# Kernel tuning notes

Measured on AMD Instinct MI355X. Metric: run time of the kernel, lower is better.

The kernel has to match this reference:

```python
import jax, jax.numpy as jnp
import numpy as np
from jax import lax

# STE sign: forward maps x>=0 -> +1, x<0 -> -1 (matches XORQuantizeSTE)
@jax.custom_vjp
def ste_sign(x):
    return jnp.where(x >= 0, jnp.ones_like(x), -jnp.ones_like(x))

def _ste_fwd(x):
    return ste_sign(x), None

def _ste_bwd(_, g):
    return (g,)  # identity pass-through

ste_sign.defvjp(_ste_fwd, _ste_bwd)


def _xor_quant(x, w):
    """Per-layer XNOR-Net quantization: alpha = mean|W| scales both
    binarized activation and binarized weight (as in the wrapper's hook
    + binarization())."""
    alpha = jnp.mean(jnp.abs(w))
    return alpha * ste_sign(x), alpha * ste_sign(w)


def _conv(x, w, b, stride):
    y = lax.conv_general_dilated(
        x, w, window_strides=(stride, stride), padding=((1, 1), (1, 1)),
        dimension_numbers=('NCHW', 'OIHW', 'NCHW'))
    return y + b[None, :, None, None]


def setup_inputs() -> dict:
    key = jax.random.key(0)
    ks = jax.random.split(key, 9)
    f32 = jnp.float32
    x = jax.random.normal(ks[0], (32, 3, 224, 224), dtype=f32)
    w1 = jax.random.normal(ks[1], (64, 3, 3, 3), dtype=f32) * 0.1
    b1 = jax.random.normal(ks[2], (64,), dtype=f32) * 0.01
    w2 = jax.random.normal(ks[3], (128, 64, 3, 3), dtype=f32) * 0.05
    b2 = jax.random.normal(ks[4], (128,), dtype=f32) * 0.01
    w3 = jax.random.normal(ks[5], (256, 128, 3, 3), dtype=f32) * 0.03
    b3 = jax.random.normal(ks[6], (256,), dtype=f32) * 0.01
    wf = jax.random.normal(ks[7], (1000, 256), dtype=f32) * 0.05
    bf = jax.random.normal(ks[8], (1000,), dtype=f32) * 0.01
    return {'x': x, 'w1': w1, 'b1': b1, 'w2': w2, 'b2': b2,
            'w3': w3, 'b3': b3, 'wf': wf, 'bf': bf}


def reference(x, w1, b1, w2, b2, w3, b3, wf, bf):
    # layer 1: binarize activation + weight with shared alpha, dense conv
    xq, wq = _xor_quant(x, w1)
    h = jnp.clip(_conv(xq, wq, b1, 2), -1.0, 1.0)   # [32,64,112,112]
    xq, wq = _xor_quant(h, w2)
    h = jnp.clip(_conv(xq, wq, b2, 2), -1.0, 1.0)   # [32,128,56,56]
    xq, wq = _xor_quant(h, w3)
    h = jnp.clip(_conv(xq, wq, b3, 2), -1.0, 1.0)   # [32,256,28,28]
    h = jnp.mean(h, axis=(2, 3))                     # global avg pool [32,256]
    xq, wq = _xor_quant(h, wf)
    return xq @ wq.T + bf                            # [32,1000]
```

## Files before the change

### kernel.cpp

```cpp
#include <hip/hip_runtime.h>
#include <stdint.h>
#include <math.h>


#define WP2_OFF    2048ull
#define WP3T_OFF   16384ull
#define WFP_OFF    65536ull
#define PART_OFF   100352ull
#define P1_OFF     102400ull
#define P2_OFF     3313664ull
#define POOLP_OFF  4919296ull

__global__ __launch_bounds__(256) void k1_conv1_pack(
    const float* __restrict__ x,  const float* __restrict__ w1, const float* __restrict__ b1,
    const float* __restrict__ w2, const float* __restrict__ w3, const float* __restrict__ wf,
    uint64_t* __restrict__ wp2, uint64_t* __restrict__ wp3t, uint64_t* __restrict__ wfp,
    double* __restrict__ part, uint64_t* __restrict__ p1)
{
    const int tid = threadIdx.x, lane = tid & 63, wid = tid >> 6, bid = blockIdx.x;
    if (bid < 896) {
        __shared__ float4   xf4[1512];
        __shared__ uint32_t xb[216];
        __shared__ uint32_t wm[64];
        __shared__ int      Ts[64];
        __shared__ double   a2s;
        const float* xf = (const float*)xf4;

        int n = bid / 28, hb = bid % 28;
        int ho0 = hb * 4;
        int hi0 = 2 * ho0 - 1;

        if (wid == 0) {
            double s = 0.0;
            #pragma unroll
            for (int i = 0; i < 27; i++) s += fabs((double)w1[lane + i*64]);
            #pragma unroll
            for (int off = 1; off < 64; off <<= 1) s += __shfl_xor(s, off, 64);
            if (lane == 0) { double a = s / 1728.0; a2s = a * a; }
        } else if (wid == 1) {
            uint32_t m = 0;
            for (int t = 0; t < 27; t++) {
                int ci = t / 9, r = t % 9, kh = r / 3, kw = r % 3;
                if (w1[((lane*3 + ci)*3 + kh)*3 + kw] >= 0.f) m |= (1u << t);
            }
            wm[lane] = m;
        }
        const float4* xg = (const float4*)x;
        for (int i = tid; i < 1512; i += 256) {
            int seg = i / 56, f4 = i % 56;
            int ci = seg / 9, r = seg % 9;
            int hi = hi0 + r;
            float4 v = make_float4(0.f, 0.f, 0.f, 0.f);
            if ((unsigned)hi < 224u) v = xg[((n*3 + ci)*224 + hi)*56 + f4];
            xf4[i] = v;
        }
        __syncthreads();
        if (tid < 64) {
            double a2 = a2s, b = (double)b1[tid];
            int k = (int)ceil(-b / a2);
            k = max(-27, min(28, k));
            while (k > -27 && (a2 * (double)(k - 1) + b >= 0.0)) k--;
            while (k <= 27 && !(a2 * (double)k + b >= 0.0)) k++;
            Ts[tid] = k;
        }
        if (tid < 189) {
            int seg = tid / 7, j = tid % 7;
            uint32_t u = 0;
            #pragma unroll
            for (int k = 0; k < 32; k++) {
                int o = (k + tid) & 31;
                if (xf[seg*224 + j*32 + o] >= 0.f) u |= (1u << o);
            }
            xb[seg*8 + j] = u;
        } else if (tid < 216) {
            xb[(tid - 189)*8 + 7] = 0u;
        }
        __syncthreads();

        for (int pass = 0; pass < 2; pass++) {
            int s = tid + pass*256;
            if (s >= 448) break;
            int dho = s / 112, wo = s % 112;
            int hop = ho0 + dho;
            uint32_t vm = 0x7FFFFFFu;
            if (hop == 0) vm &= ~0x1C0E07u;
            if (wo == 0)  vm &= ~0x1249249u;
            int c0 = 2*wo - 1;
            uint32_t xm = 0;
            if (wo > 0) {
                int w0 = c0 >> 5, sh = c0 & 31;
                #pragma unroll
                for (int ci = 0; ci < 3; ci++)
                    #pragma unroll
                    for (int kh = 0; kh < 3; kh++) {
                        int seg = ci*9 + 2*dho + kh;
                        uint64_t dw = (uint64_t)xb[seg*8 + w0]
                                    | ((uint64_t)xb[seg*8 + w0 + 1] << 32);
                        xm |= (uint32_t)((dw >> sh) & 7u) << (ci*9 + kh*3);
                    }
            } else {
                #pragma unroll
                for (int ci = 0; ci < 3; ci++)
                    #pragma unroll
                    for (int kh = 0; kh < 3; kh++) {
                        int seg = ci*9 + 2*dho + kh;
                        xm |= ((xb[seg*8] << 1) & 6u) << (ci*9 + kh*3);
                    }
            }
            int V = __popc(vm);
            uint64_t bits = 0;
            for (int co = 0; co < 64; co++) {
                int m = __popc((~(xm ^ wm[co])) & vm);
                if (2*m - V >= Ts[co]) bits |= (1ull << co);
            }
            p1[(n*112 + hop)*112 + wo] = bits;
        }
    } else {
        int rel = bid - 896;
        if (rel < 96) {
            __shared__ double sd[256];
            int t = rel >> 5, c = rel & 31;
            const float* w; int n;
            if (t == 0)      { w = w2; n = 128*64*9; }
            else if (t == 1) { w = w3; n = 256*128*9; }
            else             { w = wf; n = 1000*256; }
            int per = (n + 31) / 32;
            int lo = c * per, hi = min(n, lo + per);
            double s0 = 0.0, s1 = 0.0, s2 = 0.0, s3 = 0.0;
            int i = lo + tid;
            for (; i + 768 < hi; i += 1024) {
                s0 += fabs((double)w[i]);
                s1 += fabs((double)w[i + 256]);
                s2 += fabs((double)w[i + 512]);
                s3 += fabs((double)w[i + 768]);
            }
            for (; i < hi; i += 256) s0 += fabs((double)w[i]);
            sd[tid] = (s0 + s1) + (s2 + s3);
            __syncthreads();
            for (int off = 128; off > 0; off >>= 1) {
                if (tid < off) sd[tid] += sd[tid + off];
                __syncthreads();
            }
            if (tid == 0) part[(t + 1)*32 + c] = sd[0];
        }
        int gw = rel * 4 + wid;
        const int nw = 640;
        for (int w = gw; w < 1152; w += nw) {
            int co = w / 9, tap = w % 9, kh = tap / 3, kw = tap % 3;
            uint64_t b = __ballot(w2[((co*64 + lane)*3 + kh)*3 + kw] >= 0.f);
            if (lane == 0) wp2[w] = b;
        }
        for (int w = gw; w < 4608; w += nw) {
            int co = w / 18, r = w % 18, tap = r / 2, half = r & 1;
            int kh = tap / 3, kw = tap % 3;
            uint64_t b = __ballot(w3[((co*128 + half*64 + lane)*3 + kh)*3 + kw] >= 0.f);
            if (lane == 0) wp3t[(tap*2 + half)*256 + co] = b;
        }
        for (int w = gw; w < 4000; w += nw) {
            int o = w >> 2, j = w & 3;
            uint64_t b = __ballot(wf[o*256 + j*64 + lane] >= 0.f);
            if (lane == 0) wfp[w] = b;
        }
    }
}

__global__ __launch_bounds__(256) void k2_conv2(
    const uint64_t* __restrict__ p1, const float* __restrict__ b2,
    const double* __restrict__ part, const uint64_t* __restrict__ wp2g,
    uint32_t* __restrict__ p2)
{
    __shared__ uint64_t wp[1152];
    __shared__ uint64_t xs[1152];
    __shared__ int      M[128*4];
    const int tid = threadIdx.x, lane = tid & 63;

    for (int i = tid; i < 1152; i += 256) wp[i] = wp2g[i];
    for (int i = tid; i < 1152; i += 256) {
        int t = i >> 7, pl = i & 127;
        int pos = blockIdx.x * 128 + pl;
        int wo = pos % 56, t1 = pos / 56;
        int ho = t1 % 56, n = t1 / 56;
        int kh = t / 3, kw = t % 3;
        int hi = 2*ho + kh - 1, wi = 2*wo + kw - 1;
        bool ok = ((unsigned)hi < 112u) && ((unsigned)wi < 112u);
        xs[i] = ok ? p1[(n*112 + hi)*112 + wi] : 0ull;
    }
    __syncthreads();
    if (tid < 128) {
        int co = tid;
        double s = 0.0;
        for (int j = 0; j < 32; j++) s += part[32 + j];
        double a = s / (double)(128*64*9);
        double a2 = a * a, b = (double)b2[co];
        int k = (int)ceil(-b / a2);
        k = max(-577, min(578, k));
        while (k > -577 && (a2 * (double)(k - 1) + b >= 0.0)) k--;
        while (k <= 577 && !(a2 * (double)k + b >= 0.0)) k++;
        uint32_t P[9];
        #pragma unroll
        for (int t = 0; t < 9; t++) P[t] = __popcll(wp[co*9 + t]);
        int cT = P[0] + P[1] + P[2];
        int cL = P[0] + P[3] + P[6];
        int cC = P[0];
        #pragma unroll
        for (int cfg = 0; cfg < 4; cfg++) {
            int isT = cfg & 1, isL = (cfg >> 1) & 1;
            int V = 9 - 3*isT - 3*isL + (isT & isL);
            int corr = isT*cT + isL*cL - (isT & isL)*cC;
            int dtab = 64*V + 2*corr;
            M[co*4 + cfg] = (dtab - k) >> 1;
        }
    }
    __syncthreads();

    int q = tid >> 6;
    int co0 = q * 32;
    int pos0 = blockIdx.x * 128 + lane;
    int pos1 = pos0 + 64;
    int wo0 = pos0 % 56, ho0 = (pos0 / 56) % 56;
    int wo1 = pos1 % 56, ho1 = (pos1 / 56) % 56;
    int cfg0 = (ho0 == 0 ? 1 : 0) | (wo0 == 0 ? 2 : 0);
    int cfg1 = (ho1 == 0 ? 1 : 0) | (wo1 == 0 ? 2 : 0);
    uint64_t xv0[9], xv1[9];
    #pragma unroll
    for (int t = 0; t < 9; t++) { xv0[t] = xs[t*128 + lane]; xv1[t] = xs[t*128 + 64 + lane]; }
    uint32_t bits0 = 0, bits1 = 0;
    for (int c = 0; c < 32; c++) {
        int co = co0 + c;
        int mm0 = 0, mm1 = 0;
        #pragma unroll
        for (int t = 0; t < 9; t++) {
            uint64_t w = wp[co*9 + t];
            mm0 += __popcll(xv0[t] ^ w);
            mm1 += __popcll(xv1[t] ^ w);
        }
        if (mm0 <= M[co*4 + cfg0]) bits0 |= (1u << c);
        if (mm1 <= M[co*4 + cfg1]) bits1 |= (1u << c);
    }
    p2[pos0*4 + q] = bits0;
    p2[pos1*4 + q] = bits1;
}

__global__ __launch_bounds__(256) void k3_conv3pool(
    const uint64_t* __restrict__ p2, const float* __restrict__ b3,
    const double* __restrict__ part, const uint64_t* __restrict__ wp3t,
    double* __restrict__ partial)
{
    __shared__ uint64_t xs[28*18];
    const int tid = threadIdx.x;
    int n = blockIdx.x / 28, ho = blockIdx.x % 28;

    double s = 0.0;
    for (int j = 0; j < 32; j++) s += part[64 + j];
    double a = s / (double)(256*128*9);
    double a2 = a * a;

    uint64_t w[18];
    #pragma unroll
    for (int i = 0; i < 18; i++) w[i] = wp3t[i*256 + tid];
    uint32_t P[9];
    #pragma unroll
    for (int t = 0; t < 9; t++) P[t] = __popcll(w[2*t]) + __popcll(w[2*t+1]);

    for (int i = tid; i < 504; i += 256) {
        int wo = i / 18, r = i % 18;
        int tap = r / 2, half = r % 2;
        int kh = tap / 3, kw = tap % 3;
        int hi = 2*ho + kh - 1, wi = 2*wo + kw - 1;
        bool ok = ((unsigned)hi < 56u) && ((unsigned)wi < 56u);
        xs[i] = ok ? p2[(size_t)((n*56 + hi)*56 + wi)*2 + half] : 0ull;
    }
    __syncthreads();

    bool htop = (ho == 0);
    int rv = htop ? 2 : 3;
    double bc = (double)b3[tid];
    double sum = 0.0;
    for (int wo = 0; wo < 28; wo++) {
        int mm = 0;
        #pragma unroll
        for (int t = 0; t < 18; t++)
            mm += __popcll(xs[wo*18 + t] ^ w[t]);
        bool wl = (wo == 0);
        int cv = wl ? 2 : 3;
        int corr = 0;
        if (htop) corr += P[0] + P[1] + P[2];
        if (wl)   corr += P[0] + P[3] + P[6];
        if (htop && wl) corr -= P[0];
        int dot = 128*(rv*cv) - 2*mm + 2*corr;
        double h = a2 * (double)dot + bc;
        h = fmin(fmax(h, -1.0), 1.0);
        sum += h;
    }
    partial[(size_t)(n*28 + ho)*256 + tid] = sum;
}

__global__ __launch_bounds__(256) void k4_poolfc(
    const double* __restrict__ partial, const uint64_t* __restrict__ wfp,
    const float* __restrict__ bf, const double* __restrict__ part,
    float* __restrict__ out)
{
    __shared__ uint64_t spl[4];
    const int tid = threadIdx.x, lane = tid & 63;
    int n = blockIdx.x;
    double s = 0.0;
    for (int c = 0; c < 28; c++) s += partial[(size_t)(n*28 + c)*256 + tid];
    uint64_t bal = __ballot((s / 784.0) >= 0.0);
    if (lane == 0) spl[tid >> 6] = bal;

    double sa = 0.0;
    for (int j = 0; j < 32; j++) sa += part[96 + j];
    double a = sa / (double)(1000*256);
    double aa = a * a;
    __syncthreads();
    uint64_t s0 = spl[0], s1 = spl[1], s2 = spl[2], s3 = spl[3];
    for (int o = tid; o < 1000; o += 256) {
        int m = __popcll(s0 ^ wfp[o*4]) + __popcll(s1 ^ wfp[o*4+1])
              + __popcll(s2 ^ wfp[o*4+2]) + __popcll(s3 ^ wfp[o*4+3]);
        out[n*1000 + o] = (float)(aa * (double)(256 - 2*m) + (double)bf[o]);
    }
}

extern "C" void kernel_launch(void* const* d_in, const int* in_sizes, int n_in,
                              void* d_out, int out_size, void* d_ws, size_t ws_size,
                              hipStream_t stream) {
    const float* x  = (const float*)d_in[0];
    const float* w1 = (const float*)d_in[1];
    const float* b1 = (const float*)d_in[2];
    const float* w2 = (const float*)d_in[3];
    const float* b2 = (const float*)d_in[4];
    const float* w3 = (const float*)d_in[5];
    const float* b3 = (const float*)d_in[6];
    const float* wf = (const float*)d_in[7];
    const float* bf = (const float*)d_in[8];

    char* ws = (char*)d_ws;
    uint64_t* wp2    = (uint64_t*)(ws + WP2_OFF);
    uint64_t* wp3t   = (uint64_t*)(ws + WP3T_OFF);
    uint64_t* wfp    = (uint64_t*)(ws + WFP_OFF);
    double*   part   = (double*)  (ws + PART_OFF);
    uint64_t* p1     = (uint64_t*)(ws + P1_OFF);
    uint32_t* p2     = (uint32_t*)(ws + P2_OFF);
    double*   poolp  = (double*)  (ws + POOLP_OFF);
    float*    out    = (float*)   d_out;

    hipLaunchKernelGGL(k1_conv1_pack, dim3(1056), dim3(256), 0, stream,
                       x, w1, b1, w2, w3, wf, wp2, wp3t, wfp, part, p1);
    hipLaunchKernelGGL(k2_conv2,      dim3(784),  dim3(256), 0, stream,
                       p1, b2, part, wp2, p2);
    hipLaunchKernelGGL(k3_conv3pool,  dim3(896),  dim3(256), 0, stream,
                       (const uint64_t*)p2, b3, part, wp3t, poolp);
    hipLaunchKernelGGL(k4_poolfc,     dim3(32),   dim3(256), 0, stream,
                       poolp, wfp, bf, part, out);
}
```

Baseline: 144.5 us.

## Parallelize conv1 output channels across lanes with ballot-based bit packing

The first conv's 64-iteration per-pixel channel loop becomes a per-wave scheme. Each lane owns one output channel and keeps its weight mask and a precomputed mismatch threshold in registers, with separate thresholds for the top and left padding edges. Input masks are staged in shared memory, and each wave builds the 64-bit output word with a ballot, so one lane writes the whole row of outputs. This removes the serial per-thread channel loop and the per-iteration shared loads, at the cost of an extra barrier and only lane 0 doing the global writes.

```diff
diff --git a/kernel.cpp b/kernel.cpp
--- a/kernel.cpp
+++ b/kernel.cpp
@@ -21,8 +21,8 @@
     if (bid < 896) {
         __shared__ float4   xf4[1512];
         __shared__ uint32_t xb[216];
+        __shared__ uint32_t xms[448];
         __shared__ uint32_t wm[64];
-        __shared__ int      Ts[64];
         __shared__ double   a2s;
         const float* xf = (const float*)xf4;
 
@@ -55,14 +55,28 @@
             xf4[i] = v;
         }
         __syncthreads();
-        if (tid < 64) {
-            double a2 = a2s, b = (double)b1[tid];
+
+        uint32_t wmr = wm[lane];
+        int Mn, Ml;
+        {
+            double a2 = a2s, b = (double)b1[lane];
             int k = (int)ceil(-b / a2);
             k = max(-27, min(28, k));
             while (k > -27 && (a2 * (double)(k - 1) + b >= 0.0)) k--;
             while (k <= 27 && !(a2 * (double)k + b >= 0.0)) k++;
-            Ts[tid] = k;
-        }
+            int cntT  = __popc(wmr & 0x1C0E07u);
+            int cntL  = __popc(wmr & 0x1249249u);
+            int cntTL = __popc(wmr & 0x40201u);
+            bool topw = (hb == 0 && wid == 0);
+            if (topw) {
+                Mn = ((18 - k) >> 1) + 9 - cntT;
+                Ml = ((12 - k) >> 1) + cntL + 6 - cntT + cntTL;
+            } else {
+                Mn = (27 - k) >> 1;
+                Ml = ((18 - k) >> 1) + cntL;
+            }
+        }
+
         if (tid < 189) {
             int seg = tid / 7, j = tid % 7;
             uint32_t u = 0;
@@ -81,10 +95,6 @@
             int s = tid + pass*256;
             if (s >= 448) break;
             int dho = s / 112, wo = s % 112;
-            int hop = ho0 + dho;
-            uint32_t vm = 0x7FFFFFFu;
-            if (hop == 0) vm &= ~0x1C0E07u;
-            if (wo == 0)  vm &= ~0x1249249u;
             int c0 = 2*wo - 1;
             uint32_t xm = 0;
             if (wo > 0) {
@@ -107,13 +117,24 @@
                         xm |= ((xb[seg*8] << 1) & 6u) << (ci*9 + kh*3);
                     }
             }
-            int V = __popc(vm);
-            uint64_t bits = 0;
-            for (int co = 0; co < 64; co++) {
-                int m = __popc((~(xm ^ wm[co])) & vm);
-                if (2*m - V >= Ts[co]) bits |= (1ull << co);
-            }
-            p1[(n*112 + hop)*112 + wo] = bits;
+            xms[s] = xm;
+        }
+        __syncthreads();
+
+        {
+            int hop = ho0 + wid;
+            uint64_t* __restrict__ prow = p1 + ((size_t)(n*112 + hop))*112;
+            const uint32_t* xrow = &xms[wid*112];
+            {
+                int mm = __popc(xrow[0] ^ wmr);
+                uint64_t bal = __ballot(mm <= Ml);
+                if (lane == 0) prow[0] = bal;
+            }
+            for (int wo = 1; wo < 112; wo++) {
+                int mm = __popc(xrow[wo] ^ wmr);
+                uint64_t bal = __ballot(mm <= Mn);
+                if (lane == 0) prow[wo] = bal;
+            }
         }
     } else {
         int rel = bid - 896;
```

New measurement: 151.0 us. +4.5%, slower.
